# Kernel optimization log

Measured on AMD Instinct MI355X. Metric: run time of the kernel, lower is better.

Reference implementation:

```python
import jax, jax.numpy as jnp
import numpy as np

N = 10000      # nodes
E = 100000     # edges per direction
DIN = 128      # input feature dim (== hidden so layers stack)
H = 4          # attention heads
C = 128        # out channels per head (concat=False -> mean over heads)
ED = 16        # edge_attr dim
L = 2          # number of layers (len(hidden_sizes))
NEG_SLOPE = 0.2
EPS = 1e-5


def setup_inputs() -> dict:
    key = jax.random.key(0)
    ks = jax.random.split(key, 32)
    f32 = jnp.float32

    def nrm(k, shape, s=0.05):
        return jax.random.normal(k, shape, dtype=f32) * s

    inp = {}
    inp["x"] = nrm(ks[0], (N, DIN), 1.0)
    inp["fwd_edges_index"] = jax.random.randint(ks[1], (2, E), 0, N, dtype=jnp.int32)
    inp["bwd_edges_index"] = jax.random.randint(ks[2], (2, E), 0, N, dtype=jnp.int32)
    inp["edge_attr"] = nrm(ks[3], (E, ED), 1.0)
    # GATv2 params, stacked over layers; suffix _f = FWDGATLayer, _b = BWDGATLayer
    for i, sfx in enumerate(["f", "b"]):
        o = 4 + 7 * i
        inp[f"Wl_{sfx}"] = nrm(ks[o + 0], (L, DIN, H * C))   # lin_l (source x_j)
        inp[f"bl_{sfx}"] = jnp.zeros((L, H * C), f32)
        inp[f"Wr_{sfx}"] = nrm(ks[o + 1], (L, DIN, H * C))   # lin_r (target x_i)
        inp[f"br_{sfx}"] = jnp.zeros((L, H * C), f32)
        inp[f"We_{sfx}"] = nrm(ks[o + 2], (L, ED, H * C))    # lin_edge (no bias)
        inp[f"att_{sfx}"] = nrm(ks[o + 3], (L, H, C))        # attention vector a
        inp[f"bias_{sfx}"] = jnp.zeros((L, C), f32)          # final bias (concat=False)
    # Merge MLP: Linear(2C,C) -> ReLU -> Linear(C,C)
    inp["Wm1"] = nrm(ks[20], (L, 2 * C, C)); inp["bm1"] = jnp.zeros((L, C), f32)
    inp["Wm2"] = nrm(ks[21], (L, C, C));     inp["bm2"] = jnp.zeros((L, C), f32)
    # BatchNorm affine params (training-mode batch stats)
    inp["gamma"] = jnp.ones((L, C), f32)
    inp["beta"] = jnp.zeros((L, C), f32)
    return inp


def gatv2(x, src, dst, eattr, Wl, bl, Wr, br, We, att, bias):
    """PyG GATv2Conv, heads=H, concat=False (mean over heads), share_weights=False."""
    xl = (x @ Wl + bl).reshape(N, H, C)          # source-side transform (x_j)
    xr = (x @ Wr + br).reshape(N, H, C)          # target-side transform (x_i)
    ee = (eattr @ We).reshape(E, H, C)           # edge embedding
    z = jax.nn.leaky_relu(xl[src] + xr[dst] + ee, NEG_SLOPE)   # [E,H,C]
    logits = jnp.einsum('ehc,hc->eh', z, att)    # per-edge per-head scores
    # scatter-softmax over incoming edges of each target node
    amax = jax.lax.stop_gradient(jax.ops.segment_max(logits, dst, num_segments=N))
    amax = jnp.where(jnp.isfinite(amax), amax, 0.0)  # nodes with no in-edges
    ex = jnp.exp(logits - amax[dst])
    denom = jax.ops.segment_sum(ex, dst, num_segments=N)
    alpha = ex / denom[dst]                      # [E,H]
    msg = (xl[src] * alpha[:, :, None]).reshape(E, H * C)
    agg = jax.ops.segment_sum(msg, dst, num_segments=N).reshape(N, H, C)
    return agg.mean(axis=1) + bias               # concat=False -> head mean


def batch_norm(x, gamma, beta):
    mu = x.mean(axis=0)
    var = x.var(axis=0)  # biased var, as torch BN uses for normalization
    return gamma * (x - mu) * jax.lax.rsqrt(var + EPS) + beta


def reference(x, fwd_edges_index, bwd_edges_index, edge_attr,
              Wl_f, bl_f, Wr_f, br_f, We_f, att_f, bias_f,
              Wl_b, bl_b, Wr_b, br_b, We_b, att_b, bias_b,
              Wm1, bm1, Wm2, bm2, gamma, beta):
    fs, fd = fwd_edges_index[0], fwd_edges_index[1]
    bs, bd = bwd_edges_index[0], bwd_edges_index[1]
    h = x
    for l in range(L):
        f = gatv2(h, fs, fd, edge_attr, Wl_f[l], bl_f[l], Wr_f[l], br_f[l],
                  We_f[l], att_f[l], bias_f[l])
        b = gatv2(h, bs, bd, edge_attr, Wl_b[l], bl_b[l], Wr_b[l], br_b[l],
                  We_b[l], att_b[l], bias_b[l])
        m = jnp.concatenate([f, b], axis=1)                     # [N, 2C]
        m = jax.nn.relu(m @ Wm1[l] + bm1[l]) @ Wm2[l] + bm2[l]  # merge MLP
        h = jax.nn.relu(batch_norm(m, gamma[l], beta[l]))
    return h
```

## Files before the change

kernel.cpp:

```cpp
#include <hip/hip_runtime.h>

constexpr int N_  = 10000;
constexpr int E_  = 100000;
constexpr int HC_ = 512;
constexpr int MP_ = 10112;
constexpr float NEG_SLOPE_ = 0.2f;

typedef unsigned int u32;
typedef unsigned short u16;
typedef __attribute__((ext_vector_type(8))) short bf16x8;
typedef __attribute__((ext_vector_type(4))) float f32x4;
typedef __attribute__((ext_vector_type(2))) float f32x2;

__device__ __forceinline__ u16 f2bf(float f) {
  u32 u = __float_as_uint(f);
  u32 r = u + 0x7fffu + ((u >> 16) & 1u);
  return (u16)(r >> 16);
}
__device__ __forceinline__ float bf2f(u16 u) {
  return __uint_as_float((u32)u << 16);
}
__device__ __forceinline__ f32x2 bf2x2(u32 p) {
  return (f32x2){__uint_as_float(p << 16), __uint_as_float(p & 0xffff0000u)};
}
__device__ __forceinline__ void async16(const void* g, void* l) {
  __builtin_amdgcn_global_load_lds((const __attribute__((address_space(1))) u32*)g,
                                   (__attribute__((address_space(3))) u32*)l, 16, 0, 0);
}
__device__ __forceinline__ f32x2 fma2s(float c, f32x2 v, f32x2 acc) {
  return __builtin_elementwise_fma((f32x2){c, c}, v, acc);
}
__device__ __forceinline__ f32x2 fma2v(f32x2 a, f32x2 b, f32x2 acc) {
  return __builtin_elementwise_fma(a, b, acc);
}


__global__ void k_hist(const int* __restrict__ fdst, const int* __restrict__ bdst,
                       int* __restrict__ degf, int* __restrict__ degb) {
  int e = blockIdx.x * 256 + threadIdx.x;
  if (e < E_) {
    atomicAdd(&degf[fdst[e]], 1);
    atomicAdd(&degb[bdst[e]], 1);
  }
}

__global__ void k_scan(const int* __restrict__ degf, const int* __restrict__ degb,
                       int* __restrict__ rpf, int* __restrict__ rpb) {
  const int* deg = blockIdx.x ? degb : degf;
  int* rp = blockIdx.x ? rpb : rpf;
  const int CH = 40;
  int t = threadIdx.x;
  int base = t * CH;
  int s = 0;
  for (int i = 0; i < CH; ++i) {
    int idx = base + i;
    if (idx < N_) s += deg[idx];
  }
  __shared__ int lds[256];
  lds[t] = s;
  __syncthreads();
  for (int off = 1; off < 256; off <<= 1) {
    int v = (t >= off) ? lds[t - off] : 0;
    __syncthreads();
    lds[t] += v;
    __syncthreads();
  }
  int run = lds[t] - s;
  for (int i = 0; i < CH; ++i) {
    int idx = base + i;
    if (idx < N_) { rp[idx] = run; run += deg[idx]; }
  }
  if (t == 255) rp[N_] = lds[255];
}

__global__ void k_scatter(const int* __restrict__ src, const int* __restrict__ dst,
                          const int* __restrict__ rp, int* __restrict__ cur,
                          int* __restrict__ csrc, float* __restrict__ eP,
                          const float* __restrict__ eattr) {
  int e = blockIdx.x * 256 + threadIdx.x;
  if (e < E_) {
    int d = dst[e];
    int pos = rp[d] + atomicAdd(&cur[d], 1);
    csrc[pos] = src[e];
    const float4* s4 = reinterpret_cast<const float4*>(eattr + (size_t)e * 16);
    float4* d4 = reinterpret_cast<float4*>(eP + (size_t)pos * 16);
    d4[0] = s4[0]; d4[1] = s4[1]; d4[2] = s4[2]; d4[3] = s4[3];
  }
}


__global__ void k_wprep(const float* __restrict__ Wl_f, const float* __restrict__ Wr_f,
                        const float* __restrict__ Wl_b, const float* __restrict__ Wr_b,
                        const float* __restrict__ bl_f, const float* __restrict__ br_f,
                        const float* __restrict__ bl_b, const float* __restrict__ br_b,
                        const float* __restrict__ Wm1, const float* __restrict__ Wm2,
                        u16* __restrict__ WCATh, float* __restrict__ BCAT,
                        u16* __restrict__ WM1h, u16* __restrict__ WM2h) {
  int idx = blockIdx.x * 256 + threadIdx.x;
  if (idx < 2 * 2048 * 128) {
    int l = idx >> 18;
    int rem = idx & 262143;
    int k = rem >> 11;
  }
  if (idx < 2 * 2048 * 128) {
    int l = idx >> 18;
    int rem = idx & 262143;
    int j = rem >> 7, k = rem & 127;
    int grp = j >> 9, jj = j & 511;
    const float* W = grp == 0 ? Wl_f : grp == 1 ? Wr_f : grp == 2 ? Wl_b : Wr_b;
    WCATh[idx] = f2bf(W[((size_t)(l * 128 + k)) * 512 + jj]);
  }
  if (idx < 2 * 2048) {
    int l = idx >> 11, j = idx & 2047;
    int grp = j >> 9, jj = j & 511;
    const float* bs = grp == 0 ? bl_f : grp == 1 ? br_f : grp == 2 ? bl_b : br_b;
    BCAT[idx] = bs[l * 512 + jj];
  }
  if (idx < 2 * 128 * 256) {
    int l = idx >> 15;
    int rem = idx & 32767;
    int n = rem >> 8, k = rem & 255;
    WM1h[idx] = f2bf(Wm1[((size_t)(l * 256 + k)) * 128 + n]);
  }
  if (idx < 2 * 128 * 128) {
    int l = idx >> 14;
    int rem = idx & 16383;
    int n = rem >> 7, k = rem & 127;
    WM2h[idx] = f2bf(Wm2[((size_t)(l * 128 + k)) * 128 + n]);
  }
}

__global__ void k_cast(const float* __restrict__ x, u16* __restrict__ Xh) {
  int idx = blockIdx.x * 256 + threadIdx.x;
  if (idx >= MP_ * 32) return;
  int row = idx >> 5;
  int c4 = (idx & 31) << 2;
  ushort4 o;
  if (row < N_) {
    float4 v = *reinterpret_cast<const float4*>(x + (size_t)row * 128 + c4);
    o.x = f2bf(v.x); o.y = f2bf(v.y); o.z = f2bf(v.z); o.w = f2bf(v.w);
  } else {
    o.x = o.y = o.z = o.w = 0;
  }
  *reinterpret_cast<ushort4*>(Xh + (size_t)row * 128 + c4) = o;
}


template <int K>
__global__ __launch_bounds__(256) void k_hgemm(const u16* __restrict__ A,
                                               const u16* __restrict__ Bt,
                                               const float* __restrict__ bias,
                                               u16* __restrict__ Cb, int M, int Ncols) {
  __shared__ __align__(16) u16 As[128 * 128];
  __shared__ __align__(16) u16 Bs[128 * 128];
  const int tid = threadIdx.x;
  const int lane = tid & 63, wave = tid >> 6;
  const int l16 = lane & 15, lq = lane >> 4;
  const int wm = wave & 1, wn = wave >> 1;
  const u16* Arow0 = A + (size_t)blockIdx.y * 128 * K;
  const u16* Brow0 = Bt + (size_t)blockIdx.x * 128 * K;

  f32x4 acc[4][4];
#pragma unroll
  for (int i = 0; i < 4; ++i)
#pragma unroll
    for (int j = 0; j < 4; ++j) acc[i][j] = (f32x4){0.f, 0.f, 0.f, 0.f};

  for (int kc = 0; kc < K; kc += 128) {
    if (kc) __syncthreads();
#pragma unroll
    for (int i = 0; i < 8; ++i) {
      int rg = i * 4 + wave;
      int r = rg * 4 + (lane >> 4);
      int cc = kc + (lane & 15) * 8;
      async16(Arow0 + (size_t)r * K + cc, (char*)As + rg * 1024);
      async16(Brow0 + (size_t)r * K + cc, (char*)Bs + rg * 1024);
    }
    __syncthreads();
    const u16* Ab = As + (wm * 64 + l16) * 128 + lq * 8;
    const u16* Bb = Bs + (wn * 64 + l16) * 128 + lq * 8;
#pragma unroll
    for (int ks = 0; ks < 4; ++ks) {
      bf16x8 af[4], bfr[4];
#pragma unroll
      for (int i = 0; i < 4; ++i)
        af[i] = *reinterpret_cast<const bf16x8*>(Ab + i * 16 * 128 + ks * 32);
#pragma unroll
      for (int j = 0; j < 4; ++j)
        bfr[j] = *reinterpret_cast<const bf16x8*>(Bb + j * 16 * 128 + ks * 32);
#pragma unroll
      for (int i = 0; i < 4; ++i)
#pragma unroll
        for (int j = 0; j < 4; ++j)
          acc[i][j] = __builtin_amdgcn_mfma_f32_16x16x32_bf16(af[i], bfr[j], acc[i][j], 0, 0, 0);
    }
  }

  const int row_base = blockIdx.y * 128 + wm * 64;
  const int col_base = blockIdx.x * 128 + wn * 64;
#pragma unroll
  for (int i = 0; i < 4; ++i) {
#pragma unroll
    for (int r = 0; r < 4; ++r) {
      int row = row_base + i * 16 + lq * 4 + r;
      if (row < M) {
#pragma unroll
        for (int j = 0; j < 4; ++j) {
          int col = col_base + j * 16 + l16;
          Cb[(size_t)row * Ncols + col] = f2bf(acc[i][j][r] + bias[col]);
        }
      }
    }
  }
}


__global__ __launch_bounds__(256, 6) void k_gat(
    const u16* __restrict__ XLXRh,
    const int* __restrict__ rpf, const int* __restrict__ csf, const float* __restrict__ ePf,
    const int* __restrict__ rpb, const int* __restrict__ csb, const float* __restrict__ ePb,
    const float* __restrict__ We_f, const float* __restrict__ We_b,
    const float* __restrict__ att_f, const float* __restrict__ att_b,
    const float* __restrict__ bias_f, const float* __restrict__ bias_b,
    u16* __restrict__ FBh, int layer) {
  const int n = blockIdx.x;
  const int dir = blockIdx.y;
  const int* rp = dir ? rpb : rpf;
  const int* cs = dir ? csb : csf;
  const float* eP = dir ? ePb : ePf;
  const float* We = (dir ? We_b : We_f) + layer * 16 * HC_;
  const float* att = (dir ? att_b : att_f) + layer * HC_;
  const float* bias = (dir ? bias_b : bias_f) + layer * 128;
  const int t = threadIdx.x;
  const int ch = t << 1;
  const u16* XL = XLXRh + dir * 1024;
  const u16* XR = XL + 512;

  f32x2 a2 = *reinterpret_cast<const f32x2*>(att + ch);
  u32 xru = *reinterpret_cast<const u32*>(XR + (size_t)n * 2048 + ch);
  f32x2 xr2 = bf2x2(xru);
  f32x2 we[16];
#pragma unroll
  for (int k = 0; k < 16; ++k)
    we[k] = *reinterpret_cast<const f32x2*>(We + k * HC_ + ch);

  auto pre = [&](f32x2 x2, const float4* ep) -> float {
    float4 e0 = ep[0], e1 = ep[1], e2 = ep[2], e3 = ep[3];
    f32x2 z = x2 + xr2;
#define EE_(c, kk) z = fma2s(c, we[kk], z)
    EE_(e0.x, 0); EE_(e0.y, 1); EE_(e0.z, 2); EE_(e0.w, 3);
    EE_(e1.x, 4); EE_(e1.y, 5); EE_(e1.z, 6); EE_(e1.w, 7);
    EE_(e2.x, 8); EE_(e2.y, 9); EE_(e2.z, 10); EE_(e2.w, 11);
    EE_(e3.x, 12); EE_(e3.y, 13); EE_(e3.z, 14); EE_(e3.w, 15);
#undef EE_
    const f32x2 zz = {0.f, 0.f};
    const f32x2 ns = {NEG_SLOPE_, NEG_SLOPE_};
    f32x2 l2 = fma2v(ns, __builtin_elementwise_min(z, zz),
                     __builtin_elementwise_max(z, zz));
    f32x2 d = l2 * a2;
    return d.x + d.y;
  };

  f32x2 acc2 = {0.f, 0.f};
  float denom = 0.f;
  const int s = rp[n], epos = rp[n + 1];
  int i = s;
  for (; i + 2 <= epos; i += 2) {
    int sn0 = cs[i], sn1 = cs[i + 1];
    u32 xu0 = *reinterpret_cast<const u32*>(XL + (size_t)sn0 * 2048 + ch);
    u32 xu1 = *reinterpret_cast<const u32*>(XL + (size_t)sn1 * 2048 + ch);
    const float4* p0 = reinterpret_cast<const float4*>(eP + (size_t)i * 16);
    f32x2 x0 = bf2x2(xu0), x1 = bf2x2(xu1);
    float pA = pre(x0, p0);
    float pB = pre(x1, p0 + 4);
#pragma unroll
    for (int kk = 1; kk < 64; kk <<= 1) {
      pA += __shfl_xor(pA, kk);
      pB += __shfl_xor(pB, kk);
    }
    float ex0 = __expf(pA);
    float ex1 = __expf(pB);
    denom += ex0 + ex1;
    acc2 = fma2s(ex0, x0, fma2s(ex1, x1, acc2));
  }
  if (i < epos) {
    int sn0 = cs[i];
    u32 xu0 = *reinterpret_cast<const u32*>(XL + (size_t)sn0 * 2048 + ch);
    const float4* p0 = reinterpret_cast<const float4*>(eP + (size_t)i * 16);
    f32x2 x0 = bf2x2(xu0);
    float pA = pre(x0, p0);
#pragma unroll
    for (int kk = 1; kk < 64; kk <<= 1) pA += __shfl_xor(pA, kk);
    float ex0 = __expf(pA);
    denom += ex0;
    acc2 = fma2s(ex0, x0, acc2);
  }

  __shared__ __align__(8) float red[512];
  float inv = denom > 0.f ? 1.f / denom : 0.f;
  *reinterpret_cast<f32x2*>(&red[ch]) = acc2 * (f32x2){inv, inv};
  __syncthreads();
  if (t < 64) {
    int c = t << 1;
    f32x2 r0 = *reinterpret_cast<const f32x2*>(&red[c]);
    f32x2 r1 = *reinterpret_cast<const f32x2*>(&red[c + 128]);
    f32x2 r2 = *reinterpret_cast<const f32x2*>(&red[c + 256]);
    f32x2 r3 = *reinterpret_cast<const f32x2*>(&red[c + 384]);
    f32x2 b2 = *reinterpret_cast<const f32x2*>(bias + c);
    f32x2 o = (r0 + r1 + r2 + r3) * (f32x2){0.25f, 0.25f} + b2;
    u32 pk = ((u32)f2bf(o.y) << 16) | (u32)f2bf(o.x);
    *reinterpret_cast<u32*>(FBh + (size_t)n * 256 + dir * 128 + c) = pk;
  }
}


__global__ __launch_bounds__(256) void k_mlp(const u16* __restrict__ FBh,
                                             const u16* __restrict__ W1,
                                             const float* __restrict__ b1,
                                             const u16* __restrict__ W2,
                                             const float* __restrict__ b2,
                                             float* __restrict__ M2,
                                             float* __restrict__ STATS) {
  __shared__ __align__(16) u16 As[128 * 128];
  __shared__ __align__(16) u16 Bs[64 * 128];
  __shared__ __align__(16) u16 M1s[64 * 128];
  __shared__ float ls[256];
  const int tid = threadIdx.x;
  const int lane = tid & 63, wave = tid >> 6;
  const int l16 = lane & 15, lq = lane >> 4;
  const int mb = blockIdx.x * 64;

  const int wr = wave & 1, wc = wave >> 1;
  f32x4 acc1[4][2];
#pragma unroll
  for (int i = 0; i < 4; ++i)
#pragma unroll
    for (int j = 0; j < 2; ++j) acc1[i][j] = (f32x4){0.f, 0.f, 0.f, 0.f};

  for (int kc = 0; kc < 256; kc += 128) {
    if (kc) __syncthreads();
#pragma unroll
    for (int tI = 0; tI < 8; ++tI) {
      int rg = tI * 4 + wave;
      int r = rg * 4 + (lane >> 4);
      async16(W1 + (size_t)r * 256 + kc + (lane & 15) * 8, (char*)As + rg * 1024);
    }
#pragma unroll
    for (int tI = 0; tI < 4; ++tI) {
      int rg = tI * 4 + wave;
      int r = rg * 4 + (lane >> 4);
      async16(FBh + (size_t)(mb + r) * 256 + kc + (lane & 15) * 8, (char*)Bs + rg * 1024);
    }
    __syncthreads();
#pragma unroll
    for (int ks = 0; ks < 4; ++ks) {
      bf16x8 af[4], bfv[2];
#pragma unroll
      for (int i = 0; i < 4; ++i)
        af[i] = *reinterpret_cast<const bf16x8*>(As + (wr * 64 + i * 16 + l16) * 128 + ks * 32 + lq * 8);
#pragma unroll
      for (int j = 0; j < 2; ++j)
        bfv[j] = *reinterpret_cast<const bf16x8*>(Bs + (wc * 32 + j * 16 + l16) * 128 + ks * 32 + lq * 8);
#pragma unroll
      for (int i = 0; i < 4; ++i)
#pragma unroll
        for (int j = 0; j < 2; ++j)
          acc1[i][j] = __builtin_amdgcn_mfma_f32_16x16x32_bf16(af[i], bfv[j], acc1[i][j], 0, 0, 0);
    }
  }
  ls[tid] = 0.f;
#pragma unroll
  for (int i = 0; i < 4; ++i) {
    float4 b1v = *reinterpret_cast<const float4*>(b1 + wr * 64 + i * 16 + lq * 4);
    float bb[4] = {b1v.x, b1v.y, b1v.z, b1v.w};
#pragma unroll
    for (int j = 0; j < 2; ++j) {
      int m = wc * 32 + j * 16 + l16;
      int k2 = wr * 64 + i * 16 + lq * 4;
      ushort4 o;
      o.x = f2bf(fmaxf(acc1[i][j][0] + bb[0], 0.f));
      o.y = f2bf(fmaxf(acc1[i][j][1] + bb[1], 0.f));
      o.z = f2bf(fmaxf(acc1[i][j][2] + bb[2], 0.f));
      o.w = f2bf(fmaxf(acc1[i][j][3] + bb[3], 0.f));
      *reinterpret_cast<ushort4*>(M1s + m * 128 + k2) = o;
    }
  }
  __syncthreads();
#pragma unroll
  for (int tI = 0; tI < 8; ++tI) {
    int rg = tI * 4 + wave;
    int r = rg * 4 + (lane >> 4);
    async16(W2 + (size_t)r * 128 + (lane & 15) * 8, (char*)As + rg * 1024);
  }
  __syncthreads();

  const int wr2 = wave & 1, wc2 = wave >> 1;
  f32x4 acc2[2][4];
#pragma unroll
  for (int i = 0; i < 2; ++i)
#pragma unroll
    for (int j = 0; j < 4; ++j) acc2[i][j] = (f32x4){0.f, 0.f, 0.f, 0.f};
#pragma unroll
  for (int ks = 0; ks < 4; ++ks) {
    bf16x8 af2[2], bf2v[4];
#pragma unroll
    for (int i = 0; i < 2; ++i)
      af2[i] = *reinterpret_cast<const bf16x8*>(M1s + (wr2 * 32 + i * 16 + l16) * 128 + ks * 32 + lq * 8);
#pragma unroll
    for (int j = 0; j < 4; ++j)
      bf2v[j] = *reinterpret_cast<const bf16x8*>(As + (wc2 * 64 + j * 16 + l16) * 128 + ks * 32 + lq * 8);
#pragma unroll
    for (int i = 0; i < 2; ++i)
#pragma unroll
      for (int j = 0; j < 4; ++j)
        acc2[i][j] = __builtin_amdgcn_mfma_f32_16x16x32_bf16(af2[i], bf2v[j], acc2[i][j], 0, 0, 0);
  }

  float s1[4] = {0.f, 0.f, 0.f, 0.f}, s2[4] = {0.f, 0.f, 0.f, 0.f};
  float b2j[4];
#pragma unroll
  for (int j = 0; j < 4; ++j) b2j[j] = b2[wc2 * 64 + j * 16 + l16];
#pragma unroll
  for (int i = 0; i < 2; ++i) {
#pragma unroll
    for (int r = 0; r < 4; ++r) {
      int m = mb + wr2 * 32 + i * 16 + lq * 4 + r;
      if (m < N_) {
#pragma unroll
        for (int j = 0; j < 4; ++j) {
          float v = acc2[i][j][r] + b2j[j];
          M2[(size_t)m * 128 + wc2 * 64 + j * 16 + l16] = v;
          s1[j] += v;
          s2[j] = fmaf(v, v, s2[j]);
        }
      }
    }
  }
#pragma unroll
  for (int j = 0; j < 4; ++j) {
    int c = wc2 * 64 + j * 16 + l16;
    atomicAdd(&ls[c], s1[j]);
    atomicAdd(&ls[128 + c], s2[j]);
  }
  __syncthreads();
  if (tid < 128) {
    atomicAdd(&STATS[tid], ls[tid]);
    atomicAdd(&STATS[128 + tid], ls[128 + tid]);
  }
}


__global__ void k_bn(const float* __restrict__ m2, const float* __restrict__ stats,
                     const float* __restrict__ gamma, const float* __restrict__ beta,
                     u16* __restrict__ houth, float* __restrict__ outf) {
  int idx = blockIdx.x * 256 + threadIdx.x;
  if (idx >= N_ * 32) return;
  int n = idx >> 5;
  int c = (idx & 31) << 2;
  float4 v = *reinterpret_cast<const float4*>(m2 + (size_t)n * 128 + c);
  const float invN = 1.f / (float)N_;
  float o[4];
  float vv[4] = {v.x, v.y, v.z, v.w};
#pragma unroll
  for (int q = 0; q < 4; ++q) {
    float mu = stats[c + q] * invN;
    float var = stats[128 + c + q] * invN - mu * mu;
    float rs = rsqrtf(var + 1e-5f);
    o[q] = fmaxf(gamma[c + q] * (vv[q] - mu) * rs + beta[c + q], 0.f);
  }
  ushort4 oh;
  oh.x = f2bf(o[0]); oh.y = f2bf(o[1]); oh.z = f2bf(o[2]); oh.w = f2bf(o[3]);
  *reinterpret_cast<ushort4*>(houth + (size_t)n * 128 + c) = oh;
  if (outf) {
    float4 of = make_float4(o[0], o[1], o[2], o[3]);
    *reinterpret_cast<float4*>(outf + (size_t)n * 128 + c) = of;
  }
}


extern "C" void kernel_launch(void* const* d_in, const int* in_sizes, int n_in,
                              void* d_out, int out_size, void* d_ws, size_t ws_size,
                              hipStream_t stream) {
  (void)in_sizes; (void)n_in; (void)out_size; (void)ws_size;
  const float* x      = (const float*)d_in[0];
  const int*   fwd    = (const int*)d_in[1];
  const int*   bwd    = (const int*)d_in[2];
  const float* eattr  = (const float*)d_in[3];
  const float* Wl_f   = (const float*)d_in[4];
  const float* bl_f   = (const float*)d_in[5];
  const float* Wr_f   = (const float*)d_in[6];
  const float* br_f   = (const float*)d_in[7];
  const float* We_f   = (const float*)d_in[8];
  const float* att_f  = (const float*)d_in[9];
  const float* bias_f = (const float*)d_in[10];
  const float* Wl_b   = (const float*)d_in[11];
  const float* bl_b   = (const float*)d_in[12];
  const float* Wr_b   = (const float*)d_in[13];
  const float* br_b   = (const float*)d_in[14];
  const float* We_b   = (const float*)d_in[15];
  const float* att_b  = (const float*)d_in[16];
  const float* bias_b = (const float*)d_in[17];
  const float* Wm1    = (const float*)d_in[18];
  const float* bm1    = (const float*)d_in[19];
  const float* Wm2    = (const float*)d_in[20];
  const float* bm2    = (const float*)d_in[21];
  const float* gamma  = (const float*)d_in[22];
  const float* beta   = (const float*)d_in[23];

  char* ws = (char*)d_ws;
  size_t off = 0;
  auto take = [&](size_t bytes) -> char* {
    char* p = ws + off;
    off += (bytes + 255) & ~(size_t)255;
    return p;
  };
  u16* WCATh = (u16*)take(2ull * 2048 * 128 * 2);
  float* BCAT = (float*)take(2ull * 2048 * 4);
  u16* WM1h = (u16*)take(2ull * 128 * 256 * 2);
  u16* WM2h = (u16*)take(2ull * 128 * 128 * 2);
  u16* Xh    = (u16*)take((size_t)MP_ * 128 * 2);
  u16* HBh   = (u16*)take((size_t)MP_ * 128 * 2);
  u16* XLXRh = (u16*)take((size_t)MP_ * 2048 * 2);
  u16* FBh   = (u16*)take((size_t)MP_ * 256 * 2);
  float* M2  = (float*)take((size_t)MP_ * 128 * 4);
  int* DEGS  = (int*)take(4ull * 40192);
  float* STATS = (float*)take(2ull * 256 * 4);
  int* degf = DEGS;
  int* degb = DEGS + (40192 / 4);
  int* curf = DEGS + 2 * (40192 / 4);
  int* curb = DEGS + 3 * (40192 / 4);
  int* rpf = (int*)take((N_ + 1) * 4);
  int* rpb = (int*)take((N_ + 1) * 4);
  int* csf = (int*)take((size_t)E_ * 4);
  int* csb = (int*)take((size_t)E_ * 4);
  float* ePf = (float*)take((size_t)E_ * 16 * 4);
  float* ePb = (float*)take((size_t)E_ * 16 * 4);

  hipMemsetAsync(DEGS, 0, 4ull * 40192 + 2ull * 256 * 4, stream);
  k_wprep<<<2048, 256, 0, stream>>>(Wl_f, Wr_f, Wl_b, Wr_b, bl_f, br_f, bl_b, br_b,
                                    Wm1, Wm2, WCATh, BCAT, WM1h, WM2h);
  k_cast<<<(MP_ * 32 + 255) / 256, 256, 0, stream>>>(x, Xh);
  k_hist<<<(E_ + 255) / 256, 256, 0, stream>>>(fwd + E_, bwd + E_, degf, degb);
  k_scan<<<2, 256, 0, stream>>>(degf, degb, rpf, rpb);
  k_scatter<<<(E_ + 255) / 256, 256, 0, stream>>>(fwd, fwd + E_, rpf, curf, csf, ePf, eattr);
  k_scatter<<<(E_ + 255) / 256, 256, 0, stream>>>(bwd, bwd + E_, rpb, curb, csb, ePb, eattr);

  for (int l = 0; l < 2; ++l) {
    const u16* hin = (l == 0) ? Xh : HBh;
    k_hgemm<128><<<dim3(16, MP_ / 128), 256, 0, stream>>>(
        hin, WCATh + (size_t)l * 2048 * 128, BCAT + l * 2048, XLXRh, N_, 2048);
    k_gat<<<dim3(N_, 2), 256, 0, stream>>>(XLXRh, rpf, csf, ePf, rpb, csb, ePb,
                                           We_f, We_b, att_f, att_b, bias_f, bias_b, FBh, l);
    k_mlp<<<MP_ / 64, 256, 0, stream>>>(FBh, WM1h + (size_t)l * 128 * 256, bm1 + l * 128,
                                        WM2h + (size_t)l * 128 * 128, bm2 + l * 128, M2,
                                        STATS + l * 256);
    k_bn<<<(N_ * 32 + 255) / 256, 256, 0, stream>>>(
        M2, STATS + l * 256, gamma + l * 128, beta + l * 128, HBh,
        (l == 1) ? (float*)d_out : nullptr);
  }
}
```

Baseline: 417.1 us.

## Split GAT into MFMA edge-logit kernel and node aggregation, switch to fp16

```diff
diff --git a/kernel.cpp b/kernel.cpp
--- a/kernel.cpp
+++ b/kernel.cpp
@@ -2,36 +2,24 @@
 
 constexpr int N_  = 10000;
 constexpr int E_  = 100000;
-constexpr int HC_ = 512;
 constexpr int MP_ = 10112;
 constexpr float NEG_SLOPE_ = 0.2f;
 
 typedef unsigned int u32;
 typedef unsigned short u16;
-typedef __attribute__((ext_vector_type(8))) short bf16x8;
+typedef __attribute__((ext_vector_type(8))) _Float16 f16x8;
+typedef __attribute__((ext_vector_type(4))) _Float16 f16x4;
 typedef __attribute__((ext_vector_type(4))) float f32x4;
-typedef __attribute__((ext_vector_type(2))) float f32x2;
-
-__device__ __forceinline__ u16 f2bf(float f) {
-  u32 u = __float_as_uint(f);
-  u32 r = u + 0x7fffu + ((u >> 16) & 1u);
-  return (u16)(r >> 16);
-}
-__device__ __forceinline__ float bf2f(u16 u) {
-  return __uint_as_float((u32)u << 16);
-}
-__device__ __forceinline__ f32x2 bf2x2(u32 p) {
-  return (f32x2){__uint_as_float(p << 16), __uint_as_float(p & 0xffff0000u)};
+
+__device__ __forceinline__ u16 f2h(float f) {
+  _Float16 h = (_Float16)f;
+  u16 r;
+  __builtin_memcpy(&r, &h, 2);
+  return r;
 }
 __device__ __forceinline__ void async16(const void* g, void* l) {
   __builtin_amdgcn_global_load_lds((const __attribute__((address_space(1))) u32*)g,
                                    (__attribute__((address_space(3))) u32*)l, 16, 0, 0);
-}
-__device__ __forceinline__ f32x2 fma2s(float c, f32x2 v, f32x2 acc) {
-  return __builtin_elementwise_fma((f32x2){c, c}, v, acc);
-}
-__device__ __forceinline__ f32x2 fma2v(f32x2 a, f32x2 b, f32x2 acc) {
-  return __builtin_elementwise_fma(a, b, acc);
 }
 
 
@@ -75,16 +63,23 @@
 
 __global__ void k_scatter(const int* __restrict__ src, const int* __restrict__ dst,
                           const int* __restrict__ rp, int* __restrict__ cur,
-                          int* __restrict__ csrc, float* __restrict__ eP,
-                          const float* __restrict__ eattr) {
+                          int* __restrict__ csrc, int* __restrict__ cdst,
+                          u16* __restrict__ ePh, const float* __restrict__ eattr) {
   int e = blockIdx.x * 256 + threadIdx.x;
   if (e < E_) {
     int d = dst[e];
     int pos = rp[d] + atomicAdd(&cur[d], 1);
     csrc[pos] = src[e];
+    cdst[pos] = d;
     const float4* s4 = reinterpret_cast<const float4*>(eattr + (size_t)e * 16);
-    float4* d4 = reinterpret_cast<float4*>(eP + (size_t)pos * 16);
-    d4[0] = s4[0]; d4[1] = s4[1]; d4[2] = s4[2]; d4[3] = s4[3];
+    float4 a = s4[0], b = s4[1], c = s4[2], dd = s4[3];
+    ushort4 o0, o1, o2, o3;
+    o0.x = f2h(a.x); o0.y = f2h(a.y); o0.z = f2h(a.z); o0.w = f2h(a.w);
+    o1.x = f2h(b.x); o1.y = f2h(b.y); o1.z = f2h(b.z); o1.w = f2h(b.w);
+    o2.x = f2h(c.x); o2.y = f2h(c.y); o2.z = f2h(c.z); o2.w = f2h(c.w);
+    o3.x = f2h(dd.x); o3.y = f2h(dd.y); o3.z = f2h(dd.z); o3.w = f2h(dd.w);
+    ushort4* d4 = reinterpret_cast<ushort4*>(ePh + (size_t)pos * 16);
+    d4[0] = o0; d4[1] = o1; d4[2] = o2; d4[3] = o3;
   }
 }
 
@@ -100,15 +95,10 @@
   if (idx < 2 * 2048 * 128) {
     int l = idx >> 18;
     int rem = idx & 262143;
-    int k = rem >> 11;
-  }
-  if (idx < 2 * 2048 * 128) {
-    int l = idx >> 18;
-    int rem = idx & 262143;
     int j = rem >> 7, k = rem & 127;
     int grp = j >> 9, jj = j & 511;
     const float* W = grp == 0 ? Wl_f : grp == 1 ? Wr_f : grp == 2 ? Wl_b : Wr_b;
-    WCATh[idx] = f2bf(W[((size_t)(l * 128 + k)) * 512 + jj]);
+    WCATh[idx] = f2h(W[((size_t)(l * 128 + k)) * 512 + jj]);
   }
   if (idx < 2 * 2048) {
     int l = idx >> 11, j = idx & 2047;
@@ -120,13 +110,13 @@
     int l = idx >> 15;
     int rem = idx & 32767;
     int n = rem >> 8, k = rem & 255;
-    WM1h[idx] = f2bf(Wm1[((size_t)(l * 256 + k)) * 128 + n]);
+    WM1h[idx] = f2h(Wm1[((size_t)(l * 256 + k)) * 128 + n]);
   }
   if (idx < 2 * 128 * 128) {
     int l = idx >> 14;
     int rem = idx & 16383;
     int n = rem >> 7, k = rem & 127;
-    WM2h[idx] = f2bf(Wm2[((size_t)(l * 128 + k)) * 128 + n]);
+    WM2h[idx] = f2h(Wm2[((size_t)(l * 128 + k)) * 128 + n]);
   }
 }
 
@@ -138,7 +128,7 @@
   ushort4 o;
   if (row < N_) {
     float4 v = *reinterpret_cast<const float4*>(x + (size_t)row * 128 + c4);
-    o.x = f2bf(v.x); o.y = f2bf(v.y); o.z = f2bf(v.z); o.w = f2bf(v.w);
+    o.x = f2h(v.x); o.y = f2h(v.y); o.z = f2h(v.z); o.w = f2h(v.w);
   } else {
     o.x = o.y = o.z = o.w = 0;
   }
@@ -181,18 +171,18 @@
     const u16* Bb = Bs + (wn * 64 + l16) * 128 + lq * 8;
 #pragma unroll
     for (int ks = 0; ks < 4; ++ks) {
-      bf16x8 af[4], bfr[4];
+      f16x8 af[4], bfr[4];
 #pragma unroll
       for (int i = 0; i < 4; ++i)
-        af[i] = *reinterpret_cast<const bf16x8*>(Ab + i * 16 * 128 + ks * 32);
+        af[i] = *reinterpret_cast<const f16x8*>(Ab + i * 16 * 128 + ks * 32);
 #pragma unroll
       for (int j = 0; j < 4; ++j)
-        bfr[j] = *reinterpret_cast<const bf16x8*>(Bb + j * 16 * 128 + ks * 32);
+        bfr[j] = *reinterpret_cast<const f16x8*>(Bb + j * 16 * 128 + ks * 32);
 #pragma unroll
       for (int i = 0; i < 4; ++i)
 #pragma unroll
         for (int j = 0; j < 4; ++j)
-          acc[i][j] = __builtin_amdgcn_mfma_f32_16x16x32_bf16(af[i], bfr[j], acc[i][j], 0, 0, 0);
+          acc[i][j] = __builtin_amdgcn_mfma_f32_16x16x32_f16(af[i], bfr[j], acc[i][j], 0, 0, 0);
     }
   }
 
@@ -207,7 +197,7 @@
 #pragma unroll
         for (int j = 0; j < 4; ++j) {
           int col = col_base + j * 16 + l16;
-          Cb[(size_t)row * Ncols + col] = f2bf(acc[i][j][r] + bias[col]);
+          Cb[(size_t)row * Ncols + col] = f2h(acc[i][j][r] + bias[col]);
         }
       }
     }
@@ -215,101 +205,133 @@
 }
 
 
-__global__ __launch_bounds__(256, 6) void k_gat(
+__global__ __launch_bounds__(256) void k_elog(
     const u16* __restrict__ XLXRh,
-    const int* __restrict__ rpf, const int* __restrict__ csf, const float* __restrict__ ePf,
-    const int* __restrict__ rpb, const int* __restrict__ csb, const float* __restrict__ ePb,
+    const int* __restrict__ csf, const int* __restrict__ cdf, const u16* __restrict__ ePf,
+    const int* __restrict__ csb, const int* __restrict__ cdb, const u16* __restrict__ ePb,
     const float* __restrict__ We_f, const float* __restrict__ We_b,
     const float* __restrict__ att_f, const float* __restrict__ att_b,
+    float* __restrict__ eXf, float* __restrict__ eXb, int layer) {
+  const int dir = blockIdx.y;
+  const int* cs = dir ? csb : csf;
+  const int* cd = dir ? cdb : cdf;
+  const u16* eP = dir ? ePb : ePf;
+  const float* We = (dir ? We_b : We_f) + layer * 16 * 512;
+  const float* att = (dir ? att_b : att_f) + layer * 512;
+  float* eX = dir ? eXb : eXf;
+
+  __shared__ __align__(16) u16 WeTs[512 * 16];
+  __shared__ __align__(16) float atts[512];
+  const int tid = threadIdx.x;
+  for (int i = tid; i < 8192; i += 256)
+    WeTs[(i & 511) * 16 + (i >> 9)] = f2h(We[i]);
+  for (int i = tid; i < 512; i += 256) atts[i] = att[i];
+  __syncthreads();
+
+  const int lane = tid & 63, wave = tid >> 6;
+  const int el = lane & 15, quad = lane >> 4;
+  const int e0 = blockIdx.x * 64 + wave * 16;
+  if (e0 >= E_) return;
+  const int e = e0 + el;
+  const bool ve = e < E_;
+  const int ec = ve ? e : E_ - 1;
+  const int se = cs[ec], de = cd[ec];
+
+  f16x8 bfr = {};
+  if (quad < 2)
+    bfr = *reinterpret_cast<const f16x8*>(eP + (size_t)ec * 16 + quad * 8);
+
+  const u16* xlp = XLXRh + (size_t)se * 2048 + dir * 1024;
+  const u16* xrp = XLXRh + (size_t)de * 2048 + dir * 1024 + 512;
+
+  float psel = 0.f;
+#pragma unroll
+  for (int h = 0; h < 4; ++h) {
+    float p = 0.f;
+#pragma unroll
+    for (int jj = 0; jj < 8; ++jj) {
+      const int mt = h * 8 + jj;
+      const int chq = mt * 16 + quad * 4;
+      f16x8 afr = *reinterpret_cast<const f16x8*>(&WeTs[(mt * 16 + el) * 16 + quad * 8]);
+      f16x4 xl4 = *reinterpret_cast<const f16x4*>(xlp + chq);
+      f16x4 xr4 = *reinterpret_cast<const f16x4*>(xrp + chq);
+      f32x4 c4 = __builtin_convertvector(xl4 + xr4, f32x4);
+      f32x4 d4 = __builtin_amdgcn_mfma_f32_16x16x32_f16(afr, bfr, c4, 0, 0, 0);
+      const f32x4 zz = {0.f, 0.f, 0.f, 0.f};
+      f32x4 lk = __builtin_elementwise_max(d4, zz) +
+                 NEG_SLOPE_ * __builtin_elementwise_min(d4, zz);
+      f32x4 a4 = *reinterpret_cast<const f32x4*>(&atts[chq]);
+      p = fmaf(lk.x, a4.x, p);
+      p = fmaf(lk.y, a4.y, p);
+      p = fmaf(lk.z, a4.z, p);
+      p = fmaf(lk.w, a4.w, p);
+    }
+    p += __shfl_xor(p, 16);
+    p += __shfl_xor(p, 32);
+    psel = (quad == h) ? p : psel;
+  }
+  if (ve) eX[(size_t)e * 4 + quad] = __expf(psel);
+}
+
+
+__global__ __launch_bounds__(256, 8) void k_gagg(
+    const u16* __restrict__ XLXRh,
+    const int* __restrict__ rpf, const int* __restrict__ csf, const float* __restrict__ eXf,
+    const int* __restrict__ rpb, const int* __restrict__ csb, const float* __restrict__ eXb,
     const float* __restrict__ bias_f, const float* __restrict__ bias_b,
     u16* __restrict__ FBh, int layer) {
-  const int n = blockIdx.x;
+  const int g = threadIdx.x >> 7;
+  const int t = threadIdx.x & 127;
+  const int n = blockIdx.x * 2 + g;
   const int dir = blockIdx.y;
   const int* rp = dir ? rpb : rpf;
   const int* cs = dir ? csb : csf;
-  const float* eP = dir ? ePb : ePf;
-  const float* We = (dir ? We_b : We_f) + layer * 16 * HC_;
-  const float* att = (dir ? att_b : att_f) + layer * HC_;
+  const float* eX = dir ? eXb : eXf;
   const float* bias = (dir ? bias_b : bias_f) + layer * 128;
-  const int t = threadIdx.x;
-  const int ch = t << 1;
+  const int ch = t << 2;
+  const int h = t >> 5;
   const u16* XL = XLXRh + dir * 1024;
-  const u16* XR = XL + 512;
-
-  f32x2 a2 = *reinterpret_cast<const f32x2*>(att + ch);
-  u32 xru = *reinterpret_cast<const u32*>(XR + (size_t)n * 2048 + ch);
-  f32x2 xr2 = bf2x2(xru);
-  f32x2 we[16];
-#pragma unroll
-  for (int k = 0; k < 16; ++k)
-    we[k] = *reinterpret_cast<const f32x2*>(We + k * HC_ + ch);
-
-  auto pre = [&](f32x2 x2, const float4* ep) -> float {
-    float4 e0 = ep[0], e1 = ep[1], e2 = ep[2], e3 = ep[3];
-    f32x2 z = x2 + xr2;
-#define EE_(c, kk) z = fma2s(c, we[kk], z)
-    EE_(e0.x, 0); EE_(e0.y, 1); EE_(e0.z, 2); EE_(e0.w, 3);
-    EE_(e1.x, 4); EE_(e1.y, 5); EE_(e1.z, 6); EE_(e1.w, 7);
-    EE_(e2.x, 8); EE_(e2.y, 9); EE_(e2.z, 10); EE_(e2.w, 11);
-    EE_(e3.x, 12); EE_(e3.y, 13); EE_(e3.z, 14); EE_(e3.w, 15);
-#undef EE_
-    const f32x2 zz = {0.f, 0.f};
-    const f32x2 ns = {NEG_SLOPE_, NEG_SLOPE_};
-    f32x2 l2 = fma2v(ns, __builtin_elementwise_min(z, zz),
-                     __builtin_elementwise_max(z, zz));
-    f32x2 d = l2 * a2;
-    return d.x + d.y;
-  };
-
-  f32x2 acc2 = {0.f, 0.f};
+
+  f32x4 acc = {0.f, 0.f, 0.f, 0.f};
   float denom = 0.f;
   const int s = rp[n], epos = rp[n + 1];
   int i = s;
   for (; i + 2 <= epos; i += 2) {
-    int sn0 = cs[i], sn1 = cs[i + 1];
-    u32 xu0 = *reinterpret_cast<const u32*>(XL + (size_t)sn0 * 2048 + ch);
-    u32 xu1 = *reinterpret_cast<const u32*>(XL + (size_t)sn1 * 2048 + ch);
-    const float4* p0 = reinterpret_cast<const float4*>(eP + (size_t)i * 16);
-    f32x2 x0 = bf2x2(xu0), x1 = bf2x2(xu1);
-    float pA = pre(x0, p0);
-    float pB = pre(x1, p0 + 4);
-#pragma unroll
-    for (int kk = 1; kk < 64; kk <<= 1) {
-      pA += __shfl_xor(pA, kk);
-      pB += __shfl_xor(pB, kk);
-    }
-    float ex0 = __expf(pA);
-    float ex1 = __expf(pB);
-    denom += ex0 + ex1;
-    acc2 = fma2s(ex0, x0, fma2s(ex1, x1, acc2));
+    int s0 = cs[i], s1 = cs[i + 1];
+    f16x4 x0h = *reinterpret_cast<const f16x4*>(XL + (size_t)s0 * 2048 + ch);
+    f16x4 x1h = *reinterpret_cast<const f16x4*>(XL + (size_t)s1 * 2048 + ch);
+    float e0 = eX[(size_t)i * 4 + h];
+    float e1 = eX[(size_t)(i + 1) * 4 + h];
+    f32x4 x0 = __builtin_convertvector(x0h, f32x4);
+    f32x4 x1 = __builtin_convertvector(x1h, f32x4);
+    denom += e0 + e1;
+    acc = __builtin_elementwise_fma((f32x4){e0, e0, e0, e0}, x0, acc);
+    acc = __builtin_elementwise_fma((f32x4){e1, e1, e1, e1}, x1, acc);
   }
   if (i < epos) {
-    int sn0 = cs[i];
-    u32 xu0 = *reinterpret_cast<const u32*>(XL + (size_t)sn0 * 2048 + ch);
-    const float4* p0 = reinterpret_cast<const float4*>(eP + (size_t)i * 16);
-    f32x2 x0 = bf2x2(xu0);
-    float pA = pre(x0, p0);
-#pragma unroll
-    for (int kk = 1; kk < 64; kk <<= 1) pA += __shfl_xor(pA, kk);
-    float ex0 = __expf(pA);
-    denom += ex0;
-    acc2 = fma2s(ex0, x0, acc2);
-  }
-
-  __shared__ __align__(8) float red[512];
+    int s0 = cs[i];
+    f16x4 x0h = *reinterpret_cast<const f16x4*>(XL + (size_t)s0 * 2048 + ch);
+    float e0 = eX[(size_t)i * 4 + h];
+    f32x4 x0 = __builtin_convertvector(x0h, f32x4);
+    denom += e0;
+    acc = __builtin_elementwise_fma((f32x4){e0, e0, e0, e0}, x0, acc);
+  }
+
+  __shared__ __align__(16) float red[2][512];
   float inv = denom > 0.f ? 1.f / denom : 0.f;
-  *reinterpret_cast<f32x2*>(&red[ch]) = acc2 * (f32x2){inv, inv};
+  *reinterpret_cast<f32x4*>(&red[g][ch]) = acc * inv;
   __syncthreads();
-  if (t < 64) {
-    int c = t << 1;
-    f32x2 r0 = *reinterpret_cast<const f32x2*>(&red[c]);
-    f32x2 r1 = *reinterpret_cast<const f32x2*>(&red[c + 128]);
-    f32x2 r2 = *reinterpret_cast<const f32x2*>(&red[c + 256]);
-    f32x2 r3 = *reinterpret_cast<const f32x2*>(&red[c + 384]);
-    f32x2 b2 = *reinterpret_cast<const f32x2*>(bias + c);
-    f32x2 o = (r0 + r1 + r2 + r3) * (f32x2){0.25f, 0.25f} + b2;
-    u32 pk = ((u32)f2bf(o.y) << 16) | (u32)f2bf(o.x);
-    *reinterpret_cast<u32*>(FBh + (size_t)n * 256 + dir * 128 + c) = pk;
+  if (t < 32) {
+    int c = t << 2;
+    f32x4 r0 = *reinterpret_cast<const f32x4*>(&red[g][c]);
+    f32x4 r1 = *reinterpret_cast<const f32x4*>(&red[g][c + 128]);
+    f32x4 r2 = *reinterpret_cast<const f32x4*>(&red[g][c + 256]);
+    f32x4 r3 = *reinterpret_cast<const f32x4*>(&red[g][c + 384]);
+    f32x4 b4 = *reinterpret_cast<const f32x4*>(bias + c);
+    f32x4 o = (r0 + r1 + r2 + r3) * 0.25f + b4;
+    ushort4 oh;
+    oh.x = f2h(o.x); oh.y = f2h(o.y); oh.z = f2h(o.z); oh.w = f2h(o.w);
+    *reinterpret_cast<ushort4*>(FBh + (size_t)n * 256 + dir * 128 + c) = oh;
   }
 }
 
@@ -354,18 +376,18 @@
     __syncthreads();
 #pragma unroll
     for (int ks = 0; ks < 4; ++ks) {
-      bf16x8 af[4], bfv[2];
+      f16x8 af[4], bfv[2];
 #pragma unroll
       for (int i = 0; i < 4; ++i)
-        af[i] = *reinterpret_cast<const bf16x8*>(As + (wr * 64 + i * 16 + l16) * 128 + ks * 32 + lq * 8);
+        af[i] = *reinterpret_cast<const f16x8*>(As + (wr * 64 + i * 16 + l16) * 128 + ks * 32 + lq * 8);
 #pragma unroll
       for (int j = 0; j < 2; ++j)
-        bfv[j] = *reinterpret_cast<const bf16x8*>(Bs + (wc * 32 + j * 16 + l16) * 128 + ks * 32 + lq * 8);
+        bfv[j] = *reinterpret_cast<const f16x8*>(Bs + (wc * 32 + j * 16 + l16) * 128 + ks * 32 + lq * 8);
 #pragma unroll
       for (int i = 0; i < 4; ++i)
 #pragma unroll
         for (int j = 0; j < 2; ++j)
-          acc1[i][j] = __builtin_amdgcn_mfma_f32_16x16x32_bf16(af[i], bfv[j], acc1[i][j], 0, 0, 0);
+          acc1[i][j] = __builtin_amdgcn_mfma_f32_16x16x32_f16(af[i], bfv[j], acc1[i][j], 0, 0, 0);
     }
   }
   ls[tid] = 0.f;
@@ -378,10 +400,10 @@
       int m = wc * 32 + j * 16 + l16;
       int k2 = wr * 64 + i * 16 + lq * 4;
       ushort4 o;
-      o.x = f2bf(fmaxf(acc1[i][j][0] + bb[0], 0.f));
-      o.y = f2bf(fmaxf(acc1[i][j][1] + bb[1], 0.f));
-      o.z = f2bf(fmaxf(acc1[i][j][2] + bb[2], 0.f));
-      o.w = f2bf(fmaxf(acc1[i][j][3] + bb[3], 0.f));
+      o.x = f2h(fmaxf(acc1[i][j][0] + bb[0], 0.f));
+      o.y = f2h(fmaxf(acc1[i][j][1] + bb[1], 0.f));
+      o.z = f2h(fmaxf(acc1[i][j][2] + bb[2], 0.f));
+      o.w = f2h(fmaxf(acc1[i][j][3] + bb[3], 0.f));
       *reinterpret_cast<ushort4*>(M1s + m * 128 + k2) = o;
     }
   }
@@ -402,18 +424,18 @@
     for (int j = 0; j < 4; ++j) acc2[i][j] = (f32x4){0.f, 0.f, 0.f, 0.f};
 #pragma unroll
   for (int ks = 0; ks < 4; ++ks) {
-    bf16x8 af2[2], bf2v[4];
+    f16x8 af2[2], bf2v[4];
 #pragma unroll
     for (int i = 0; i < 2; ++i)
-      af2[i] = *reinterpret_cast<const bf16x8*>(M1s + (wr2 * 32 + i * 16 + l16) * 128 + ks * 32 + lq * 8);
+      af2[i] = *reinterpret_cast<const f16x8*>(M1s + (wr2 * 32 + i * 16 + l16) * 128 + ks * 32 + lq * 8);
 #pragma unroll
     for (int j = 0; j < 4; ++j)
-      bf2v[j] = *reinterpret_cast<const bf16x8*>(As + (wc2 * 64 + j * 16 + l16) * 128 + ks * 32 + lq * 8);
+      bf2v[j] = *reinterpret_cast<const f16x8*>(As + (wc2 * 64 + j * 16 + l16) * 128 + ks * 32 + lq * 8);
 #pragma unroll
     for (int i = 0; i < 2; ++i)
 #pragma unroll
       for (int j = 0; j < 4; ++j)
-        acc2[i][j] = __builtin_amdgcn_mfma_f32_16x16x32_bf16(af2[i], bf2v[j], acc2[i][j], 0, 0, 0);
+        acc2[i][j] = __builtin_amdgcn_mfma_f32_16x16x32_f16(af2[i], bf2v[j], acc2[i][j], 0, 0, 0);
   }
 
   float s1[4] = {0.f, 0.f, 0.f, 0.f}, s2[4] = {0.f, 0.f, 0.f, 0.f};
@@ -469,7 +491,7 @@
     o[q] = fmaxf(gamma[c + q] * (vv[q] - mu) * rs + beta[c + q], 0.f);
   }
   ushort4 oh;
-  oh.x = f2bf(o[0]); oh.y = f2bf(o[1]); oh.z = f2bf(o[2]); oh.w = f2bf(o[3]);
+  oh.x = f2h(o[0]); oh.y = f2h(o[1]); oh.z = f2h(o[2]); oh.w = f2h(o[3]);
   *reinterpret_cast<ushort4*>(houth + (size_t)n * 128 + c) = oh;
   if (outf) {
     float4 of = make_float4(o[0], o[1], o[2], o[3]);
@@ -533,8 +555,12 @@
   int* rpb = (int*)take((N_ + 1) * 4);
   int* csf = (int*)take((size_t)E_ * 4);
   int* csb = (int*)take((size_t)E_ * 4);
-  float* ePf = (float*)take((size_t)E_ * 16 * 4);
-  float* ePb = (float*)take((size_t)E_ * 16 * 4);
+  int* cdf = (int*)take((size_t)E_ * 4);
+  int* cdb = (int*)take((size_t)E_ * 4);
+  u16* ePf = (u16*)take((size_t)E_ * 16 * 2 + 256);
+  u16* ePb = (u16*)take((size_t)E_ * 16 * 2 + 256);
+  float* eXf = (float*)take((size_t)E_ * 4 * 4);
+  float* eXb = (float*)take((size_t)E_ * 4 * 4);
 
   hipMemsetAsync(DEGS, 0, 4ull * 40192 + 2ull * 256 * 4, stream);
   k_wprep<<<2048, 256, 0, stream>>>(Wl_f, Wr_f, Wl_b, Wr_b, bl_f, br_f, bl_b, br_b,
@@ -542,15 +568,17 @@
   k_cast<<<(MP_ * 32 + 255) / 256, 256, 0, stream>>>(x, Xh);
   k_hist<<<(E_ + 255) / 256, 256, 0, stream>>>(fwd + E_, bwd + E_, degf, degb);
   k_scan<<<2, 256, 0, stream>>>(degf, degb, rpf, rpb);
-  k_scatter<<<(E_ + 255) / 256, 256, 0, stream>>>(fwd, fwd + E_, rpf, curf, csf, ePf, eattr);
-  k_scatter<<<(E_ + 255) / 256, 256, 0, stream>>>(bwd, bwd + E_, rpb, curb, csb, ePb, eattr);
+  k_scatter<<<(E_ + 255) / 256, 256, 0, stream>>>(fwd, fwd + E_, rpf, curf, csf, cdf, ePf, eattr);
+  k_scatter<<<(E_ + 255) / 256, 256, 0, stream>>>(bwd, bwd + E_, rpb, curb, csb, cdb, ePb, eattr);
 
   for (int l = 0; l < 2; ++l) {
     const u16* hin = (l == 0) ? Xh : HBh;
     k_hgemm<128><<<dim3(16, MP_ / 128), 256, 0, stream>>>(
         hin, WCATh + (size_t)l * 2048 * 128, BCAT + l * 2048, XLXRh, N_, 2048);
-    k_gat<<<dim3(N_, 2), 256, 0, stream>>>(XLXRh, rpf, csf, ePf, rpb, csb, ePb,
-                                           We_f, We_b, att_f, att_b, bias_f, bias_b, FBh, l);
+    k_elog<<<dim3((E_ + 63) / 64, 2), 256, 0, stream>>>(
+        XLXRh, csf, cdf, ePf, csb, cdb, ePb, We_f, We_b, att_f, att_b, eXf, eXb, l);
+    k_gagg<<<dim3(N_ / 2, 2), 256, 0, stream>>>(
+        XLXRh, rpf, csf, eXf, rpb, csb, eXb, bias_f, bias_b, FBh, l);
     k_mlp<<<MP_ / 64, 256, 0, stream>>>(FBh, WM1h + (size_t)l * 128 * 256, bm1 + l * 128,
                                         WM2h + (size_t)l * 128 * 128, bm2 + l * 128, M2,
                                         STATS + l * 256);
```

New measurement: 456.7 us. 1.1x slower.
